# Kernel tuning notes

Measured on AMD Instinct MI355X. Metric: run time of the kernel, lower is better.

## Reference

```python
import jax, jax.numpy as jnp
import numpy as np

EPS = 1e-5

def setup_inputs() -> dict:
    key = jax.random.key(0)
    k1, k2, k3 = jax.random.split(key, 3)
    B, P, N, Cin, Cout = 16384, 32, 2, 9, 64
    pillars = jax.random.normal(k1, (B, P, N, Cin), dtype=jnp.float32)
    num_points_per_pillar = jax.random.randint(k2, (B, P), 0, N, dtype=jnp.int32)
    # nn.Linear(9, 64, bias=False): weight (out, in), kaiming-uniform-ish init
    W = jax.random.normal(k3, (Cout, Cin), dtype=jnp.float32) * (1.0 / np.sqrt(Cin))
    gamma = jnp.ones((Cout,), dtype=jnp.float32)
    beta = jnp.zeros((Cout,), dtype=jnp.float32)
    return {"pillars": pillars, "num_points_per_pillar": num_points_per_pillar,
            "W": W, "gamma": gamma, "beta": beta}

def reference(pillars, num_points_per_pillar, W, gamma, beta):
    # pillars: (B, P, N, Cin) -> linear (no bias) -> (B, P, N, Cout)
    B, P, N, _ = pillars.shape
    x = jnp.einsum('bpnc,oc->bpno', pillars, W)
    # permute(0,3,1,2): (B, Cout, P, N)
    x = jnp.transpose(x, (0, 3, 1, 2))
    C = x.shape[1]
    # BatchNorm1d(64) applied to (B*C, P*N); requires P*N == 64.
    # Training mode: batch stats over dim 0, biased variance.
    x2 = x.reshape(B * C, P * N)
    mean = jnp.mean(x2, axis=0)            # (P*N,) == (64,)
    var = jnp.mean(jnp.square(x2 - mean), axis=0)
    x2 = (x2 - mean) * jax.lax.rsqrt(var + EPS) * gamma + beta
    x = jax.nn.relu(x2).reshape(B, C, P, N)
    # max over the point dim N -> (B, C, P)
    return jnp.max(x, axis=3)
```

## Files before the change

kernel.cpp:

```cpp
#include <hip/hip_runtime.h>


#define EPS_BN 1e-5f

__global__ __launch_bounds__(64) void pfn_prep(const float* __restrict__ W,
                                               float* __restrict__ ws) {
    __shared__ float prod[64][90];
    const int o = threadIdx.x;
    float w[9];
#pragma unroll
    for (int c = 0; c < 9; ++c) w[c] = W[o * 9 + c];
#pragma unroll
    for (int c = 0; c < 9; ++c)
#pragma unroll
        for (int c2 = 0; c2 < 9; ++c2) prod[o][c * 9 + c2] = w[c] * w[c2];
#pragma unroll
    for (int c = 0; c < 9; ++c) prod[o][81 + c] = w[c];
#pragma unroll
    for (int k = 0; k < 16; ++k) ws[96 + o * 16 + k] = 0.f;
    __syncthreads();
    for (int col = o; col < 90; col += 64) {
        float s = 0.f;
        for (int r = 0; r < 64; ++r) s += prod[r][col];
        ws[col] = s;
    }
}

__global__ __launch_bounds__(256) void pfn_stats(const float* __restrict__ pillars,
                                                 const float* __restrict__ gw,
                                                 float* __restrict__ acc8,
                                                 int npairs) {
    const int tid = threadIdx.x;
    const int lane = tid & 63;
    const int p = lane & 31;
    const int bsub = lane >> 5;

    float G[81], wsum[9];
#pragma unroll
    for (int k = 0; k < 81; ++k) G[k] = gw[k];
#pragma unroll
    for (int c = 0; c < 9; ++c) wsum[c] = gw[81 + c];

    float a1_0 = 0.f, a2_0 = 0.f;
    float a1_1 = 0.f, a2_1 = 0.f;

    const int wid = blockIdx.x * 4 + (tid >> 6);
    const int nw = gridDim.x * 4;
    for (int pr = wid; pr < npairs; pr += nw) {
        const float2* src =
            (const float2*)(pillars + (size_t)(pr * 2 + bsub) * 576 + p * 18);
        float v[18];
#pragma unroll
        for (int k = 0; k < 9; ++k) {
            const float2 t = src[k];
            v[2 * k] = t.x;
            v[2 * k + 1] = t.y;
        }
        float d0 = 0.f, d1 = 0.f, q0 = 0.f, q1 = 0.f;
#pragma unroll
        for (int c = 0; c < 9; ++c) {
            d0 = fmaf(wsum[c], v[c], d0);
            d1 = fmaf(wsum[c], v[9 + c], d1);
            float t0 = 0.f, t1 = 0.f;
#pragma unroll
            for (int c2 = 0; c2 < 9; ++c2) {
                const float g = G[c * 9 + c2];
                t0 = fmaf(g, v[c2], t0);
                t1 = fmaf(g, v[9 + c2], t1);
            }
            q0 = fmaf(v[c], t0, q0);
            q1 = fmaf(v[9 + c], t1, q1);
        }
        a1_0 += d0; a2_0 += q0;
        a1_1 += d1; a2_1 += q1;
    }

    __shared__ float red[256][5];
    red[tid][0] = a1_0; red[tid][1] = a2_0;
    red[tid][2] = a1_1; red[tid][3] = a2_1;
    __syncthreads();
    if (tid < 32) {
        float s0 = 0.f, s1 = 0.f, s2 = 0.f, s3 = 0.f;
#pragma unroll
        for (int k = 0; k < 8; ++k) {
            s0 += red[tid + 32 * k][0];
            s1 += red[tid + 32 * k][1];
            s2 += red[tid + 32 * k][2];
            s3 += red[tid + 32 * k][3];
        }
        float* acc = acc8 + (blockIdx.x & 7) * 128;
        atomicAdd(&acc[(2 * tid) * 2], s0);
        atomicAdd(&acc[(2 * tid) * 2 + 1], s1);
        atomicAdd(&acc[(2 * tid + 1) * 2], s2);
        atomicAdd(&acc[(2 * tid + 1) * 2 + 1], s3);
    }
}

__global__ __launch_bounds__(64) void pfn_finalize(const float* __restrict__ gamma,
                                                   const float* __restrict__ beta,
                                                   float* __restrict__ ws,
                                                   float invBC) {
    const int j = threadIdx.x;
    float s1 = 0.f, s2 = 0.f;
#pragma unroll
    for (int s = 0; s < 8; ++s) {
        s1 += ws[96 + s * 128 + j * 2];
        s2 += ws[96 + s * 128 + j * 2 + 1];
    }
    const float mean = s1 * invBC;
    const float var = s2 * invBC - mean * mean;
    const float a = rsqrtf(var + EPS_BN) * gamma[j];
    const float bb = beta[j] - mean * a;
    ws[1120 + j] = a;
    ws[1184 + j] = bb;
}

__global__ __launch_bounds__(256) void pfn_main(const float* __restrict__ pillars,
                                                const float* __restrict__ W,
                                                const float* __restrict__ ws,
                                                float* __restrict__ out,
                                                int npairs) {
    __shared__ float smW[64 * 12];
    const int tid = threadIdx.x;
    for (int i = tid; i < 576; i += 256) smW[(i / 9) * 12 + (i % 9)] = W[i];

    const int lane = tid & 63;
    const int p = lane & 31;
    const int bsub = lane >> 5;
    const float a0 = ws[1120 + 2 * p], a1 = ws[1120 + 2 * p + 1];
    const float b0 = ws[1184 + 2 * p], b1 = ws[1184 + 2 * p + 1];
    __syncthreads();

    const int pr = blockIdx.x * 4 + (tid >> 6);
    if (pr >= npairs) return;
    const int b = pr * 2 + bsub;

    float v[18];
    const float2* src = (const float2*)(pillars + (size_t)b * 576 + p * 18);
#pragma unroll
    for (int k = 0; k < 9; ++k) {
        const float2 t = src[k];
        v[2 * k] = t.x;
        v[2 * k + 1] = t.y;
    }

    float* Ob = out + (size_t)b * 2048 + p;
#pragma unroll 4
    for (int o = 0; o < 64; ++o) {
        float x0 = 0.f, x1 = 0.f;
#pragma unroll
        for (int c = 0; c < 9; ++c) {
            const float w = smW[o * 12 + c];
            x0 = fmaf(w, v[c], x0);
            x1 = fmaf(w, v[9 + c], x1);
        }
        const float r0 = fmaxf(fmaf(x0, a0, b0), 0.f);
        const float r1 = fmaxf(fmaf(x1, a1, b1), 0.f);
        Ob[o * 32] = fmaxf(r0, r1);
    }
}

extern "C" void kernel_launch(void* const* d_in, const int* in_sizes, int n_in,
                              void* d_out, int out_size, void* d_ws, size_t ws_size,
                              hipStream_t stream) {
    const float* pillars = (const float*)d_in[0];
    const float* W = (const float*)d_in[2];
    const float* gamma = (const float*)d_in[3];
    const float* beta = (const float*)d_in[4];
    float* out = (float*)d_out;
    float* ws = (float*)d_ws;

    const int B = in_sizes[0] / 576;
    const int npairs = B / 2;

    pfn_prep<<<1, 64, 0, stream>>>(W, ws);
    pfn_stats<<<1024, 256, 0, stream>>>(pillars, ws, ws + 96, npairs);
    pfn_finalize<<<1, 64, 0, stream>>>(gamma, beta, ws, 1.0f / ((float)B * 64.0f));
    pfn_main<<<2048, 256, 0, stream>>>(pillars, W, ws, out, npairs);
}
```

Measured before the change: 187.6 us.

## Stage pillar tiles in LDS with coalesced float4 loads and fold finalize into main

Both the stats and main kernels now load each block's 8-pillar tile into shared memory with coalesced float4 reads, then read per-thread float2 slices from LDS instead of strided global loads. The stats kernel drops its grid-stride loop and register-held Gram matrix in favour of one tile per block with the matrix in shared memory. The BN finalize kernel is removed, and every main block recomputes the scale and shift from the accumulators. Main also uses vectorized weight reads, unroll 8 and nontemporal stores. The cost is more blocks issuing atomics in stats, redundant finalize work per main block, and the assumption that B is a multiple of 8.

```diff
diff --git a/kernel.cpp b/kernel.cpp
--- a/kernel.cpp
+++ b/kernel.cpp
@@ -29,55 +29,56 @@
 __global__ __launch_bounds__(256) void pfn_stats(const float* __restrict__ pillars,
                                                  const float* __restrict__ gw,
                                                  float* __restrict__ acc8,
-                                                 int npairs) {
+                                                 int ntiles) {
+    __shared__ float4 smP4[1152];
+    __shared__ float smG[96];
+    __shared__ float red[256][5];
+    float* smP = (float*)smP4;
+
     const int tid = threadIdx.x;
+    const int b_base4 = blockIdx.x * 1152;
+    const float4* P4 = (const float4*)pillars;
+
+#pragma unroll
+    for (int i = tid; i < 1152; i += 256) smP4[i] = P4[b_base4 + i];
+    if (tid < 90) smG[tid] = gw[tid];
+    __syncthreads();
+
     const int lane = tid & 63;
     const int p = lane & 31;
     const int bsub = lane >> 5;
+    const int b_local = (tid >> 6) * 2 + bsub;
 
-    float G[81], wsum[9];
-#pragma unroll
-    for (int k = 0; k < 81; ++k) G[k] = gw[k];
-#pragma unroll
-    for (int c = 0; c < 9; ++c) wsum[c] = gw[81 + c];
-
-    float a1_0 = 0.f, a2_0 = 0.f;
-    float a1_1 = 0.f, a2_1 = 0.f;
-
-    const int wid = blockIdx.x * 4 + (tid >> 6);
-    const int nw = gridDim.x * 4;
-    for (int pr = wid; pr < npairs; pr += nw) {
-        const float2* src =
-            (const float2*)(pillars + (size_t)(pr * 2 + bsub) * 576 + p * 18);
-        float v[18];
+    float v[18];
+    {
+        const float2* src = (const float2*)&smP[b_local * 576 + p * 18];
 #pragma unroll
         for (int k = 0; k < 9; ++k) {
             const float2 t = src[k];
             v[2 * k] = t.x;
             v[2 * k + 1] = t.y;
         }
-        float d0 = 0.f, d1 = 0.f, q0 = 0.f, q1 = 0.f;
-#pragma unroll
-        for (int c = 0; c < 9; ++c) {
-            d0 = fmaf(wsum[c], v[c], d0);
-            d1 = fmaf(wsum[c], v[9 + c], d1);
-            float t0 = 0.f, t1 = 0.f;
-#pragma unroll
-            for (int c2 = 0; c2 < 9; ++c2) {
-                const float g = G[c * 9 + c2];
-                t0 = fmaf(g, v[c2], t0);
-                t1 = fmaf(g, v[9 + c2], t1);
-            }
-            q0 = fmaf(v[c], t0, q0);
-            q1 = fmaf(v[9 + c], t1, q1);
-        }
-        a1_0 += d0; a2_0 += q0;
-        a1_1 += d1; a2_1 += q1;
     }
 
-    __shared__ float red[256][5];
-    red[tid][0] = a1_0; red[tid][1] = a2_0;
-    red[tid][2] = a1_1; red[tid][3] = a2_1;
+    float d0 = 0.f, d1 = 0.f, q0 = 0.f, q1 = 0.f;
+#pragma unroll
+    for (int c = 0; c < 9; ++c) {
+        const float wc = smG[81 + c];
+        d0 = fmaf(wc, v[c], d0);
+        d1 = fmaf(wc, v[9 + c], d1);
+        float t0 = 0.f, t1 = 0.f;
+#pragma unroll
+        for (int c2 = 0; c2 < 9; ++c2) {
+            const float g = smG[c * 9 + c2];
+            t0 = fmaf(g, v[c2], t0);
+            t1 = fmaf(g, v[9 + c2], t1);
+        }
+        q0 = fmaf(v[c], t0, q0);
+        q1 = fmaf(v[9 + c], t1, q1);
+    }
+
+    red[tid][0] = d0; red[tid][1] = q0;
+    red[tid][2] = d1; red[tid][3] = q1;
     __syncthreads();
     if (tid < 32) {
         float s0 = 0.f, s1 = 0.f, s2 = 0.f, s3 = 0.f;
@@ -96,67 +97,79 @@
     }
 }
 
-__global__ __launch_bounds__(64) void pfn_finalize(const float* __restrict__ gamma,
-                                                   const float* __restrict__ beta,
-                                                   float* __restrict__ ws,
-                                                   float invBC) {
-    const int j = threadIdx.x;
-    float s1 = 0.f, s2 = 0.f;
-#pragma unroll
-    for (int s = 0; s < 8; ++s) {
-        s1 += ws[96 + s * 128 + j * 2];
-        s2 += ws[96 + s * 128 + j * 2 + 1];
-    }
-    const float mean = s1 * invBC;
-    const float var = s2 * invBC - mean * mean;
-    const float a = rsqrtf(var + EPS_BN) * gamma[j];
-    const float bb = beta[j] - mean * a;
-    ws[1120 + j] = a;
-    ws[1184 + j] = bb;
-}
-
 __global__ __launch_bounds__(256) void pfn_main(const float* __restrict__ pillars,
                                                 const float* __restrict__ W,
-                                                const float* __restrict__ ws,
+                                                const float* __restrict__ acc8,
+                                                const float* __restrict__ gamma,
+                                                const float* __restrict__ beta,
                                                 float* __restrict__ out,
-                                                int npairs) {
+                                                float invBC, int ntiles) {
+    __shared__ float4 smP4[1152];
     __shared__ float smW[64 * 12];
+    __shared__ float smAB[128];
+    float* smP = (float*)smP4;
+
     const int tid = threadIdx.x;
+    const int b_base4 = blockIdx.x * 1152;
+    const float4* P4 = (const float4*)pillars;
+
+#pragma unroll
+    for (int i = tid; i < 1152; i += 256) smP4[i] = P4[b_base4 + i];
     for (int i = tid; i < 576; i += 256) smW[(i / 9) * 12 + (i % 9)] = W[i];
+    if (tid < 64) {
+        const int j = tid;
+        float s1 = 0.f, s2 = 0.f;
+#pragma unroll
+        for (int s = 0; s < 8; ++s) {
+            s1 += acc8[s * 128 + j * 2];
+            s2 += acc8[s * 128 + j * 2 + 1];
+        }
+        const float mean = s1 * invBC;
+        const float var = s2 * invBC - mean * mean;
+        const float a = rsqrtf(var + EPS_BN) * gamma[j];
+        smAB[j] = a;
+        smAB[64 + j] = beta[j] - mean * a;
+    }
+    __syncthreads();
 
     const int lane = tid & 63;
     const int p = lane & 31;
     const int bsub = lane >> 5;
-    const float a0 = ws[1120 + 2 * p], a1 = ws[1120 + 2 * p + 1];
-    const float b0 = ws[1184 + 2 * p], b1 = ws[1184 + 2 * p + 1];
-    __syncthreads();
-
-    const int pr = blockIdx.x * 4 + (tid >> 6);
-    if (pr >= npairs) return;
-    const int b = pr * 2 + bsub;
+    const int b_local = (tid >> 6) * 2 + bsub;
+    const int b = blockIdx.x * 8 + b_local;
 
     float v[18];
-    const float2* src = (const float2*)(pillars + (size_t)b * 576 + p * 18);
+    {
+        const float2* src = (const float2*)&smP[b_local * 576 + p * 18];
 #pragma unroll
-    for (int k = 0; k < 9; ++k) {
-        const float2 t = src[k];
-        v[2 * k] = t.x;
-        v[2 * k + 1] = t.y;
+        for (int k = 0; k < 9; ++k) {
+            const float2 t = src[k];
+            v[2 * k] = t.x;
+            v[2 * k + 1] = t.y;
+        }
     }
+    const float a0 = smAB[2 * p], a1 = smAB[2 * p + 1];
+    const float b0 = smAB[64 + 2 * p], b1 = smAB[64 + 2 * p + 1];
 
     float* Ob = out + (size_t)b * 2048 + p;
-#pragma unroll 4
+#pragma unroll 8
     for (int o = 0; o < 64; ++o) {
+        const float4 w0 = *(const float4*)&smW[o * 12];
+        const float4 w1 = *(const float4*)&smW[o * 12 + 4];
+        const float wc8 = smW[o * 12 + 8];
         float x0 = 0.f, x1 = 0.f;
-#pragma unroll
-        for (int c = 0; c < 9; ++c) {
-            const float w = smW[o * 12 + c];
-            x0 = fmaf(w, v[c], x0);
-            x1 = fmaf(w, v[9 + c], x1);
-        }
+        x0 = fmaf(w0.x, v[0], x0); x1 = fmaf(w0.x, v[9], x1);
+        x0 = fmaf(w0.y, v[1], x0); x1 = fmaf(w0.y, v[10], x1);
+        x0 = fmaf(w0.z, v[2], x0); x1 = fmaf(w0.z, v[11], x1);
+        x0 = fmaf(w0.w, v[3], x0); x1 = fmaf(w0.w, v[12], x1);
+        x0 = fmaf(w1.x, v[4], x0); x1 = fmaf(w1.x, v[13], x1);
+        x0 = fmaf(w1.y, v[5], x0); x1 = fmaf(w1.y, v[14], x1);
+        x0 = fmaf(w1.z, v[6], x0); x1 = fmaf(w1.z, v[15], x1);
+        x0 = fmaf(w1.w, v[7], x0); x1 = fmaf(w1.w, v[16], x1);
+        x0 = fmaf(wc8, v[8], x0);  x1 = fmaf(wc8, v[17], x1);
         const float r0 = fmaxf(fmaf(x0, a0, b0), 0.f);
         const float r1 = fmaxf(fmaf(x1, a1, b1), 0.f);
-        Ob[o * 32] = fmaxf(r0, r1);
+        __builtin_nontemporal_store(fmaxf(r0, r1), &Ob[o * 32]);
     }
 }
 
@@ -171,10 +184,10 @@
     float* ws = (float*)d_ws;
 
     const int B = in_sizes[0] / 576;
-    const int npairs = B / 2;
+    const int ntiles = B / 8;
 
     pfn_prep<<<1, 64, 0, stream>>>(W, ws);
-    pfn_stats<<<1024, 256, 0, stream>>>(pillars, ws, ws + 96, npairs);
-    pfn_finalize<<<1, 64, 0, stream>>>(gamma, beta, ws, 1.0f / ((float)B * 64.0f));
-    pfn_main<<<2048, 256, 0, stream>>>(pillars, W, ws, out, npairs);
+    pfn_stats<<<ntiles, 256, 0, stream>>>(pillars, ws, ws + 96, ntiles);
+    pfn_main<<<ntiles, 256, 0, stream>>>(pillars, W, ws + 96, gamma, beta, out,
+                                         1.0f / ((float)B * 64.0f), ntiles);
 }
```

Result: slower. 204.9 us (+9.2%).
